# Performance work log

Measured on AMD Instinct MI355X. Metric: run time of the kernel, lower is better.

Reference implementation:

```python
import jax, jax.numpy as jnp
import numpy as np

L, B, E, H = 2048, 4, 1024, 8
D1 = 2 * E  # expand_ratio * embed_dim, already divisible by H
EPS = 1e-8


def setup_inputs() -> dict:
    key = jax.random.key(0)
    ks = jax.random.split(key, 12)
    std = 0.02
    return {
        "query": jax.random.normal(ks[0], (L, B, E), jnp.float32),
        "key": jax.random.normal(ks[1], (L, B, E), jnp.float32),
        "value": jax.random.normal(ks[2], (L, B, E), jnp.float32),
        "u_w": jax.random.normal(ks[3], (D1, E), jnp.float32) * std,
        "u_b": jax.random.normal(ks[4], (D1,), jnp.float32) * std,
        "v_w": jax.random.normal(ks[5], (D1, E), jnp.float32) * std,
        "v_b": jax.random.normal(ks[6], (D1,), jnp.float32) * std,
        "o_w": jax.random.normal(ks[7], (E, D1), jnp.float32) * std,
        "o_b": jax.random.normal(ks[8], (E,), jnp.float32) * std,
        # Toeplitz relative-position coefficients: t_0 (zero), t_1..t_{n-1} (pos), t_{-1}..t_{-(n-1)} (neg)
        "pos": jax.random.normal(ks[9], (H, L - 1), jnp.float32) * std,
        "zero": jax.random.normal(ks[10], (H, 1), jnp.float32) * std,
        "neg": jax.random.normal(ks[11], (H, L - 1), jnp.float32) * std,
    }


def _toeplitz_mix(v, pos, zero, neg):
    # v: (b, h, n, d). y_i = sum_j t_{i-j} v_j via circular conv of length 2n.
    b, h, n, d = v.shape
    m = 2 * n
    # a[0]=t_0, a[1:n]=t_1..t_{n-1}, a[n]=0 (unused), a[n+1:2n]=t_{-(n-1)}..t_{-1}
    a = jnp.concatenate([zero, pos[:, : n - 1], jnp.zeros((h, 1), v.dtype), neg[:, : n - 1][:, ::-1]], axis=-1)
    af = jnp.fft.rfft(a, n=m, axis=-1)            # (h, n+1)
    vf = jnp.fft.rfft(v, n=m, axis=-2)            # (b, h, n+1, d)
    y = jnp.fft.irfft(af[None, :, :, None] * vf, n=m, axis=-2)
    return y[:, :, :n, :]


def reference(query, key, value, u_w, u_b, v_w, v_b, o_w, o_b, pos, zero, neg):
    n, b, e = query.shape
    # SimpleRMSNorm: x / (||x||_2 / sqrt(d) + eps)
    rms = jnp.linalg.norm(query, axis=-1, keepdims=True) * (e ** -0.5)
    x = query / (rms + EPS)
    u = jax.nn.silu(jnp.einsum("nbe,fe->nbf", x, u_w) + u_b)   # (n, b, d1)
    v = jax.nn.silu(jnp.einsum("nbe,fe->nbf", x, v_w) + v_b)   # (n, b, d1)
    hd = v.shape[-1] // H
    vh = v.reshape(n, b, H, hd).transpose(1, 2, 0, 3)          # (b, h, n, d)
    y = _toeplitz_mix(vh, pos, zero, neg)                      # (b, h, n, d)
    y = y.transpose(2, 0, 1, 3).reshape(n, b, H * hd)          # (n, b, d1)
    out = u * y
    return jnp.einsum("nbf,ef->nbe", out, o_w) + o_b + query
```

## Files before the change

### kernel.cpp

```cpp
#include <hip/hip_runtime.h>
#include <math.h>

typedef unsigned short u16;
typedef __bf16 bf16x8 __attribute__((ext_vector_type(8)));
typedef float f32x4 __attribute__((ext_vector_type(4)));

#define LSEQ 2048
#define NB   4
#define NE   1024
#define NHEAD 8
#define ND1  2048
#define NHD  256
#define NM   8192
#define CRP  4104

__device__ __forceinline__ u16 f2bf(float f) {
  unsigned u = __float_as_uint(f);
  u += 0x7FFFu + ((u >> 16) & 1u);
  return (u16)(u >> 16);
}
__device__ __forceinline__ float bf2f(u16 h) {
  return __uint_as_float(((unsigned)h) << 16);
}

__device__ __forceinline__ void gl_lds16(const u16* g, u16* l) {
  __builtin_amdgcn_global_load_lds(
      (const __attribute__((address_space(1))) void*)g,
      (__attribute__((address_space(3))) void*)l, 16, 0, 0);
}

__global__ __launch_bounds__(256) void cvt_kernel(const float* __restrict__ src,
                                                  u16* __restrict__ dst, int n4) {
  int i = blockIdx.x * 256 + threadIdx.x;
  if (i < n4) {
    float4 v = ((const float4*)src)[i];
    ushort4 o;
    o.x = f2bf(v.x); o.y = f2bf(v.y); o.z = f2bf(v.z); o.w = f2bf(v.w);
    ((ushort4*)dst)[i] = o;
  }
}

__global__ __launch_bounds__(256) void build_cr8(const float* __restrict__ pos,
                                                 const float* __restrict__ zero,
                                                 const float* __restrict__ neg,
                                                 u16* __restrict__ cr8) {
  int h = blockIdx.x >> 3, s = blockIdx.x & 7;
  u16* out = cr8 + (size_t)blockIdx.x * CRP;
  for (int m = threadIdx.x; m < CRP; m += 256) {
    int mm = m + s;
    float val = 0.f;
    if (mm <= 4094) {
      int t = 2047 - mm;
      if (t == 0)      val = zero[h];
      else if (t > 0)  val = pos[h * (LSEQ - 1) + t - 1];
      else             val = neg[h * (LSEQ - 1) + (-t) - 1];
    }
    out[m] = f2bf(val);
  }
}

__global__ __launch_bounds__(256) void rmsnorm_kernel(const float* __restrict__ q,
                                                      u16* __restrict__ x) {
  int row = blockIdx.x;
  float4 v = ((const float4*)(q + (size_t)row * NE))[threadIdx.x];
  float ss = v.x * v.x + v.y * v.y + v.z * v.z + v.w * v.w;
  #pragma unroll
  for (int off = 32; off > 0; off >>= 1) ss += __shfl_down(ss, off, 64);
  __shared__ float wss[4];
  int wave = threadIdx.x >> 6, lane = threadIdx.x & 63;
  if (lane == 0) wss[wave] = ss;
  __syncthreads();
  float tot = wss[0] + wss[1] + wss[2] + wss[3];
  float scale = 1.f / (sqrtf(tot) * 0.03125f + 1e-8f);
  ushort4 o;
  o.x = f2bf(v.x * scale); o.y = f2bf(v.y * scale);
  o.z = f2bf(v.z * scale); o.w = f2bf(v.w * scale);
  ((ushort4*)(x + (size_t)row * NE))[threadIdx.x] = o;
}

__global__ __launch_bounds__(256) void transpose_v(const u16* __restrict__ v,
                                                   u16* __restrict__ vT) {
  __shared__ u16 s[64 * 66];
  int j0 = blockIdx.x * 64, d0 = blockIdx.y * 64;
  int h = blockIdx.z >> 2, b = blockIdx.z & 3;
  #pragma unroll
  for (int it = 0; it < 16; ++it) {
    int idx = threadIdx.x + 256 * it;
    int r = idx >> 6, c = idx & 63;
    s[r * 66 + c] = v[((size_t)(j0 + r) * NB + b) * ND1 + h * NHD + d0 + c];
  }
  __syncthreads();
  #pragma unroll
  for (int it = 0; it < 16; ++it) {
    int idx = threadIdx.x + 256 * it;
    int r = idx >> 6, c = idx & 63;
    vT[((size_t)h * (NB * NHD) + b * NHD + d0 + r) * LSEQ + j0 + c] = s[c * 66 + r];
  }
}

template <int MODE>
__global__ __launch_bounds__(256) void gemm_kernel(
    const u16* __restrict__ A, const u16* __restrict__ Bw,
    const float* __restrict__ bias, const float* __restrict__ resid,
    u16* __restrict__ Cbf, float* __restrict__ Cf,
    int Msz, int Nsz, int Ksz) {
  __shared__ __align__(16) u16 As[128 * 64];
  __shared__ __align__(16) u16 Ws[128 * 64];

  const int tid = threadIdx.x;
  const int lane = tid & 63, wave = tid >> 6;
  const int wr = (wave >> 1) * 64, wc = (wave & 1) * 64;
  const int lr = lane & 15, lq = lane >> 4;
  const int i0 = blockIdx.y * 128, n0 = blockIdx.x * 128;

  const u16* Bh = Bw;
  const u16* Acr = A;
  if (MODE == 1) {
    Bh  = Bw + (size_t)blockIdx.z * Nsz * Ksz;
    Acr = A + (size_t)blockIdx.z * 8 * CRP;
  }

  f32x4 acc[4][4];
  #pragma unroll
  for (int a = 0; a < 4; ++a)
    #pragma unroll
    for (int b = 0; b < 4; ++b) acc[a][b] = (f32x4){0.f, 0.f, 0.f, 0.f};

  const int nkt = Ksz >> 6;
  for (int kt = 0; kt < nkt; ++kt) {
    #pragma unroll
    for (int it = 0; it < 4; ++it) {
      int vv = tid + 256 * it;
      int r = vv >> 3, c8 = vv & 7;
      int c8s = c8 ^ (r & 7);
      const u16* src;
      if (MODE != 1) {
        src = A + (size_t)(i0 + r) * Ksz + kt * 64 + c8s * 8;
      } else {
        int p = 2047 - (i0 + r) + kt * 64;
        int s = p & 7, qq = p - s;
        src = Acr + (size_t)s * CRP + qq + c8s * 8;
      }
      gl_lds16(src, &As[(size_t)(wave * 64 + it * 256) * 8]);
    }
    #pragma unroll
    for (int it = 0; it < 4; ++it) {
      int vv = tid + 256 * it;
      int r = vv >> 3, c8 = vv & 7;
      int c8s = c8 ^ (r & 7);
      gl_lds16(Bh + (size_t)(n0 + r) * Ksz + kt * 64 + c8s * 8,
               &Ws[(size_t)(wave * 64 + it * 256) * 8]);
    }
    __syncthreads();
    #pragma unroll
    for (int ks = 0; ks < 2; ++ks) {
      bf16x8 af[4], bfr[4];
      #pragma unroll
      for (int rt = 0; rt < 4; ++rt) {
        int ar = wr + rt * 16 + lr;
        int cq = (ks * 4 + lq) ^ (ar & 7);
        af[rt] = *(const bf16x8*)&As[ar * 64 + cq * 8];
      }
      #pragma unroll
      for (int ct = 0; ct < 4; ++ct) {
        int br = wc + ct * 16 + lr;
        int cq = (ks * 4 + lq) ^ (br & 7);
        bfr[ct] = *(const bf16x8*)&Ws[br * 64 + cq * 8];
      }
      #pragma unroll
      for (int rt = 0; rt < 4; ++rt)
        #pragma unroll
        for (int ct = 0; ct < 4; ++ct)
          acc[rt][ct] = __builtin_amdgcn_mfma_f32_16x16x32_bf16(
              af[rt], bfr[ct], acc[rt][ct], 0, 0, 0);
    }
    __syncthreads();
  }

  #pragma unroll
  for (int rt = 0; rt < 4; ++rt) {
    #pragma unroll
    for (int ct = 0; ct < 4; ++ct) {
      int col = n0 + wc + ct * 16 + lr;
      #pragma unroll
      for (int reg = 0; reg < 4; ++reg) {
        int row = i0 + wr + rt * 16 + lq * 4 + reg;
        float yv = acc[rt][ct][reg];
        if (MODE == 0) {
          float t = yv + bias[col];
          t = t / (1.f + __expf(-t));
          Cbf[(size_t)row * Nsz + col] = f2bf(t);
        } else if (MODE == 1) {
          int b = col >> 8, d = col & 255;
          size_t ui = ((size_t)row * NB + b) * ND1 + (size_t)blockIdx.z * NHD + d;
          float uv = bf2f(Cbf[ui]);
          Cbf[ui] = f2bf(uv * yv);
        } else {
          size_t oi = (size_t)row * Nsz + col;
          Cf[oi] = yv + bias[col] + resid[oi];
        }
      }
    }
  }
}

extern "C" void kernel_launch(void* const* d_in, const int* in_sizes, int n_in,
                              void* d_out, int out_size, void* d_ws, size_t ws_size,
                              hipStream_t stream) {
  const float* q    = (const float*)d_in[0];
  const float* uw   = (const float*)d_in[3];
  const float* ub   = (const float*)d_in[4];
  const float* vw   = (const float*)d_in[5];
  const float* vb   = (const float*)d_in[6];
  const float* ow   = (const float*)d_in[7];
  const float* ob   = (const float*)d_in[8];
  const float* pos  = (const float*)d_in[9];
  const float* zero = (const float*)d_in[10];
  const float* neg  = (const float*)d_in[11];
  float* out = (float*)d_out;

  char* ws = (char*)d_ws;
  u16* x   = (u16*)(ws + 0);
  u16* uwb = (u16*)(ws + 16777216);
  u16* vwb = (u16*)(ws + 20971520);
  u16* owb = (u16*)(ws + 25165824);
  u16* u   = (u16*)(ws + 29360128);
  u16* v   = (u16*)(ws + 62914560);
  u16* vT  = (u16*)(ws + 96468992);
  u16* cr8 = (u16*)(ws + 130023424);

  cvt_kernel<<<2048, 256, 0, stream>>>(uw, uwb, 524288);
  cvt_kernel<<<2048, 256, 0, stream>>>(vw, vwb, 524288);
  cvt_kernel<<<2048, 256, 0, stream>>>(ow, owb, 524288);
  build_cr8<<<64, 256, 0, stream>>>(pos, zero, neg, cr8);
  rmsnorm_kernel<<<NM, 256, 0, stream>>>(q, x);

  gemm_kernel<0><<<dim3(16, 64, 1), 256, 0, stream>>>(x, uwb, ub, nullptr, u, nullptr,
                                                      NM, ND1, NE);
  gemm_kernel<0><<<dim3(16, 64, 1), 256, 0, stream>>>(x, vwb, vb, nullptr, v, nullptr,
                                                      NM, ND1, NE);
  transpose_v<<<dim3(32, 4, 32), 256, 0, stream>>>(v, vT);
  gemm_kernel<1><<<dim3(8, 16, 8), 256, 0, stream>>>(cr8, vT, nullptr, nullptr, u, nullptr,
                                                     LSEQ, NB * NHD, LSEQ);
  gemm_kernel<2><<<dim3(8, 64, 1), 256, 0, stream>>>(u, owb, ob, q, nullptr, out,
                                                     NM, NE, ND1);
}
```

Before: 407.6 us.

## Add 256x256 double-buffered 8-wave GEMM with phased MFMA/load interleave

```diff
diff --git a/kernel.cpp b/kernel.cpp
--- a/kernel.cpp
+++ b/kernel.cpp
@@ -98,6 +98,199 @@
   }
 }
 
+
+__device__ __forceinline__ bf16x8 ldsfrag(const u16* buf, int rr, int q) {
+  return *(const bf16x8*)(buf + rr * 64 + ((q ^ (rr & 7)) * 8));
+}
+
+template <int MODE>
+__device__ __forceinline__ void stage_Ah(const u16* A, const u16* Acr, int Ksz,
+                                         int i0, int kt, int half, u16* dstbuf,
+                                         int tid) {
+  int wave = tid >> 6;
+  #pragma unroll
+  for (int it = 0; it < 2; ++it) {
+    int vv = it * 512 + tid;
+    int r = vv >> 3, c8 = vv & 7, c8s = c8 ^ (r & 7);
+    int row = i0 + half * 128 + r;
+    const u16* src;
+    if (MODE != 1) {
+      src = A + (size_t)row * Ksz + kt * 64 + c8s * 8;
+    } else {
+      int p = 2047 - row + kt * 64;
+      int s = p & 7, qq = p - s;
+      src = Acr + (size_t)s * CRP + qq + c8s * 8;
+    }
+    gl_lds16(src, dstbuf + half * 8192 + (it * 512 + wave * 64) * 8);
+  }
+}
+
+__device__ __forceinline__ void stage_Bh(const u16* B, int Ksz, int n0, int kt,
+                                         int half, u16* dstbuf, int tid) {
+  int wave = tid >> 6;
+  #pragma unroll
+  for (int it = 0; it < 2; ++it) {
+    int vv = it * 512 + tid;
+    int r = vv >> 3, c8 = vv & 7, c8s = c8 ^ (r & 7);
+    gl_lds16(B + (size_t)(n0 + half * 128 + r) * Ksz + kt * 64 + c8s * 8,
+             dstbuf + half * 8192 + (it * 512 + wave * 64) * 8);
+  }
+}
+
+#define PHASE_MID()                                        \
+  __builtin_amdgcn_s_barrier();                            \
+  asm volatile("s_waitcnt lgkmcnt(0)" ::: "memory");       \
+  __builtin_amdgcn_sched_barrier(0);                       \
+  __builtin_amdgcn_s_setprio(1);
+
+#define PHASE_END()                                        \
+  __builtin_amdgcn_s_setprio(0);                           \
+  __builtin_amdgcn_s_barrier();                            \
+  __builtin_amdgcn_sched_barrier(0);
+
+template <int MODE>
+__global__ __launch_bounds__(512, 2) void gemm256(
+    const u16* __restrict__ A, const u16* __restrict__ Bw,
+    const float* __restrict__ bias, u16* __restrict__ Cbf,
+    int Msz, int Nsz, int Ksz) {
+  extern __shared__ __align__(16) u16 lds[];
+  u16* As = lds;
+  u16* Ws = lds + 32768;
+
+  const int tid = threadIdx.x;
+  const int lane = tid & 63, wave = tid >> 6;
+  const int wr = (wave >> 2) * 128, wc = (wave & 3) * 64;
+  const int lr = lane & 15, lq = lane >> 4;
+  const int i0 = blockIdx.y * 256, n0 = blockIdx.x * 256;
+
+  const u16* Bh = Bw;
+  const u16* Acr = A;
+  if (MODE == 1) {
+    Bh  = Bw + (size_t)blockIdx.z * Nsz * Ksz;
+    Acr = A + (size_t)blockIdx.z * 8 * CRP;
+  }
+  const int nkt = Ksz >> 6;
+
+  f32x4 acc[8][4];
+  #pragma unroll
+  for (int a = 0; a < 8; ++a)
+    #pragma unroll
+    for (int b = 0; b < 4; ++b) acc[a][b] = (f32x4){0.f, 0.f, 0.f, 0.f};
+
+  stage_Ah<MODE>(A, Acr, Ksz, i0, 0, 0, As, tid);
+  stage_Ah<MODE>(A, Acr, Ksz, i0, 0, 1, As, tid);
+  stage_Bh(Bh, Ksz, n0, 0, 0, Ws, tid);
+  stage_Bh(Bh, Ksz, n0, 0, 1, Ws, tid);
+  stage_Bh(Bh, Ksz, n0, 1, 0, Ws + 16384, tid);
+  stage_Bh(Bh, Ksz, n0, 1, 1, Ws + 16384, tid);
+  asm volatile("s_waitcnt vmcnt(4)" ::: "memory");
+  __builtin_amdgcn_s_barrier();
+  __builtin_amdgcn_sched_barrier(0);
+
+  for (int tt = 0; tt < nkt; ++tt) {
+    const int cur = tt & 1;
+    const u16* Ab = As + cur * 16384;
+    const u16* Wb = Ws + cur * 16384;
+    u16* An = As + (cur ^ 1) * 16384;
+    u16* Wn = Ws + cur * 16384;
+
+    bf16x8 a[4][2], b[2][2], b2[2][2];
+
+    #pragma unroll
+    for (int rt = 0; rt < 4; ++rt) {
+      int ar = wr + rt * 16 + lr;
+      a[rt][0] = ldsfrag(Ab, ar, lq);
+      a[rt][1] = ldsfrag(Ab, ar, 4 + lq);
+    }
+    #pragma unroll
+    for (int ct = 0; ct < 2; ++ct) {
+      int br = wc + ct * 16 + lr;
+      b[ct][0] = ldsfrag(Wb, br, lq);
+      b[ct][1] = ldsfrag(Wb, br, 4 + lq);
+    }
+    if (tt + 1 < nkt) stage_Ah<MODE>(A, Acr, Ksz, i0, tt + 1, 0, An, tid);
+    PHASE_MID();
+    #pragma unroll
+    for (int rt = 0; rt < 4; ++rt)
+      #pragma unroll
+      for (int ct = 0; ct < 2; ++ct) {
+        acc[rt][ct] = __builtin_amdgcn_mfma_f32_16x16x32_bf16(a[rt][0], b[ct][0], acc[rt][ct], 0, 0, 0);
+        acc[rt][ct] = __builtin_amdgcn_mfma_f32_16x16x32_bf16(a[rt][1], b[ct][1], acc[rt][ct], 0, 0, 0);
+      }
+    PHASE_END();
+
+    #pragma unroll
+    for (int ct = 0; ct < 2; ++ct) {
+      int br = wc + (ct + 2) * 16 + lr;
+      b2[ct][0] = ldsfrag(Wb, br, lq);
+      b2[ct][1] = ldsfrag(Wb, br, 4 + lq);
+    }
+    if (tt + 1 < nkt) stage_Ah<MODE>(A, Acr, Ksz, i0, tt + 1, 1, An, tid);
+    PHASE_MID();
+    #pragma unroll
+    for (int rt = 0; rt < 4; ++rt)
+      #pragma unroll
+      for (int ct = 0; ct < 2; ++ct) {
+        acc[rt][ct + 2] = __builtin_amdgcn_mfma_f32_16x16x32_bf16(a[rt][0], b2[ct][0], acc[rt][ct + 2], 0, 0, 0);
+        acc[rt][ct + 2] = __builtin_amdgcn_mfma_f32_16x16x32_bf16(a[rt][1], b2[ct][1], acc[rt][ct + 2], 0, 0, 0);
+      }
+    PHASE_END();
+
+    #pragma unroll
+    for (int rt = 0; rt < 4; ++rt) {
+      int ar = wr + (rt + 4) * 16 + lr;
+      a[rt][0] = ldsfrag(Ab, ar, lq);
+      a[rt][1] = ldsfrag(Ab, ar, 4 + lq);
+    }
+    if (tt + 2 < nkt) stage_Bh(Bh, Ksz, n0, tt + 2, 0, Wn, tid);
+    PHASE_MID();
+    #pragma unroll
+    for (int rt = 0; rt < 4; ++rt)
+      #pragma unroll
+      for (int ct = 0; ct < 2; ++ct) {
+        acc[rt + 4][ct + 2] = __builtin_amdgcn_mfma_f32_16x16x32_bf16(a[rt][0], b2[ct][0], acc[rt + 4][ct + 2], 0, 0, 0);
+        acc[rt + 4][ct + 2] = __builtin_amdgcn_mfma_f32_16x16x32_bf16(a[rt][1], b2[ct][1], acc[rt + 4][ct + 2], 0, 0, 0);
+      }
+    PHASE_END();
+
+    if (tt + 2 < nkt) stage_Bh(Bh, Ksz, n0, tt + 2, 1, Wn, tid);
+    if (tt == nkt - 2) { asm volatile("s_waitcnt vmcnt(0)" ::: "memory"); }
+    else               { asm volatile("s_waitcnt vmcnt(4)" ::: "memory"); }
+    PHASE_MID();
+    #pragma unroll
+    for (int rt = 0; rt < 4; ++rt)
+      #pragma unroll
+      for (int ct = 0; ct < 2; ++ct) {
+        acc[rt + 4][ct] = __builtin_amdgcn_mfma_f32_16x16x32_bf16(a[rt][0], b[ct][0], acc[rt + 4][ct], 0, 0, 0);
+        acc[rt + 4][ct] = __builtin_amdgcn_mfma_f32_16x16x32_bf16(a[rt][1], b[ct][1], acc[rt + 4][ct], 0, 0, 0);
+      }
+    PHASE_END();
+  }
+
+  #pragma unroll
+  for (int rt = 0; rt < 8; ++rt) {
+    #pragma unroll
+    for (int ct = 0; ct < 4; ++ct) {
+      int col = n0 + wc + ct * 16 + lr;
+      #pragma unroll
+      for (int reg = 0; reg < 4; ++reg) {
+        int row = i0 + wr + rt * 16 + lq * 4 + reg;
+        float yv = acc[rt][ct][reg];
+        if (MODE == 0) {
+          float t = yv + bias[col];
+          t = t / (1.f + __expf(-t));
+          Cbf[(size_t)row * Nsz + col] = f2bf(t);
+        } else {
+          int b = col >> 8, d = col & 255;
+          size_t ui = ((size_t)row * NB + b) * ND1 + (size_t)blockIdx.z * NHD + d;
+          float uv = bf2f(Cbf[ui]);
+          Cbf[ui] = f2bf(uv * yv);
+        }
+      }
+    }
+  }
+}
+
 template <int MODE>
 __global__ __launch_bounds__(256) void gemm_kernel(
     const u16* __restrict__ A, const u16* __restrict__ Bw,
@@ -113,13 +306,6 @@
   const int lr = lane & 15, lq = lane >> 4;
   const int i0 = blockIdx.y * 128, n0 = blockIdx.x * 128;
 
-  const u16* Bh = Bw;
-  const u16* Acr = A;
-  if (MODE == 1) {
-    Bh  = Bw + (size_t)blockIdx.z * Nsz * Ksz;
-    Acr = A + (size_t)blockIdx.z * 8 * CRP;
-  }
-
   f32x4 acc[4][4];
   #pragma unroll
   for (int a = 0; a < 4; ++a)
@@ -133,22 +319,15 @@
       int vv = tid + 256 * it;
       int r = vv >> 3, c8 = vv & 7;
       int c8s = c8 ^ (r & 7);
-      const u16* src;
-      if (MODE != 1) {
-        src = A + (size_t)(i0 + r) * Ksz + kt * 64 + c8s * 8;
-      } else {
-        int p = 2047 - (i0 + r) + kt * 64;
-        int s = p & 7, qq = p - s;
-        src = Acr + (size_t)s * CRP + qq + c8s * 8;
-      }
-      gl_lds16(src, &As[(size_t)(wave * 64 + it * 256) * 8]);
+      gl_lds16(A + (size_t)(i0 + r) * Ksz + kt * 64 + c8s * 8,
+               &As[(size_t)(wave * 64 + it * 256) * 8]);
     }
     #pragma unroll
     for (int it = 0; it < 4; ++it) {
       int vv = tid + 256 * it;
       int r = vv >> 3, c8 = vv & 7;
       int c8s = c8 ^ (r & 7);
-      gl_lds16(Bh + (size_t)(n0 + r) * Ksz + kt * 64 + c8s * 8,
+      gl_lds16(Bw + (size_t)(n0 + r) * Ksz + kt * 64 + c8s * 8,
                &Ws[(size_t)(wave * 64 + it * 256) * 8]);
     }
     __syncthreads();
@@ -186,19 +365,8 @@
       for (int reg = 0; reg < 4; ++reg) {
         int row = i0 + wr + rt * 16 + lq * 4 + reg;
         float yv = acc[rt][ct][reg];
-        if (MODE == 0) {
-          float t = yv + bias[col];
-          t = t / (1.f + __expf(-t));
-          Cbf[(size_t)row * Nsz + col] = f2bf(t);
-        } else if (MODE == 1) {
-          int b = col >> 8, d = col & 255;
-          size_t ui = ((size_t)row * NB + b) * ND1 + (size_t)blockIdx.z * NHD + d;
-          float uv = bf2f(Cbf[ui]);
-          Cbf[ui] = f2bf(uv * yv);
-        } else {
-          size_t oi = (size_t)row * Nsz + col;
-          Cf[oi] = yv + bias[col] + resid[oi];
-        }
+        size_t oi = (size_t)row * Nsz + col;
+        Cf[oi] = yv + bias[col] + resid[oi];
       }
     }
   }
@@ -229,18 +397,21 @@
   u16* vT  = (u16*)(ws + 96468992);
   u16* cr8 = (u16*)(ws + 130023424);
 
+  hipFuncSetAttribute((const void*)gemm256<0>,
+                      hipFuncAttributeMaxDynamicSharedMemorySize, 131072);
+  hipFuncSetAttribute((const void*)gemm256<1>,
+                      hipFuncAttributeMaxDynamicSharedMemorySize, 131072);
+
   cvt_kernel<<<2048, 256, 0, stream>>>(uw, uwb, 524288);
   cvt_kernel<<<2048, 256, 0, stream>>>(vw, vwb, 524288);
   cvt_kernel<<<2048, 256, 0, stream>>>(ow, owb, 524288);
   build_cr8<<<64, 256, 0, stream>>>(pos, zero, neg, cr8);
   rmsnorm_kernel<<<NM, 256, 0, stream>>>(q, x);
 
-  gemm_kernel<0><<<dim3(16, 64, 1), 256, 0, stream>>>(x, uwb, ub, nullptr, u, nullptr,
-                                                      NM, ND1, NE);
-  gemm_kernel<0><<<dim3(16, 64, 1), 256, 0, stream>>>(x, vwb, vb, nullptr, v, nullptr,
-                                                      NM, ND1, NE);
+  gemm256<0><<<dim3(8, 32, 1), 512, 131072, stream>>>(x, uwb, ub, u, NM, ND1, NE);
+  gemm256<0><<<dim3(8, 32, 1), 512, 131072, stream>>>(x, vwb, vb, v, NM, ND1, NE);
   transpose_v<<<dim3(32, 4, 32), 256, 0, stream>>>(v, vT);
-  gemm_kernel<1><<<dim3(8, 16, 8), 256, 0, stream>>>(cr8, vT, nullptr, nullptr, u, nullptr,
+  gemm256<1><<<dim3(4, 8, 8), 512, 131072, stream>>>(cr8, vT, nullptr, u,
                                                      LSEQ, NB * NHD, LSEQ);
   gemm_kernel<2><<<dim3(8, 64, 1), 256, 0, stream>>>(u, owb, ob, q, nullptr, out,
                                                      NM, NE, ND1);
```

After: 373.2 us. 8.5% less time.
